# Kernel optimization log

Hardware: AMD Instinct MI355X
Metric: run time of the kernel (lower is better)

## Reference

```python
import jax, jax.numpy as jnp
import numpy as np

N = 50000   # num nodes
E = 800000  # num edges
D = 128     # in_features
C = 1.0     # curvature c
MIN_NORM = 1e-15
BALL_EPS = 4e-3  # float32 boundary eps in PoincareBall.proj


def setup_inputs() -> dict:
    key = jax.random.key(0)
    k1, k2 = jax.random.split(key)
    x = jax.random.normal(k1, (N, D), dtype=jnp.float32)
    edge_index = jax.random.randint(k2, (2, E), 0, N, dtype=jnp.int32)
    return {"x": x, "edge_index": edge_index}


def _expmap0(u, c):
    sqrt_c = c ** 0.5
    u_norm = jnp.maximum(jnp.linalg.norm(u, axis=-1, keepdims=True), MIN_NORM)
    return jnp.tanh(sqrt_c * u_norm) * u / (sqrt_c * u_norm)


def _proj(p, c):
    norm = jnp.maximum(jnp.linalg.norm(p, axis=-1, keepdims=True), MIN_NORM)
    maxnorm = (1.0 - BALL_EPS) / (c ** 0.5)
    return jnp.where(norm > maxnorm, p / norm * maxnorm, p)


def reference(x, edge_index):
    row, col = edge_index[0], edge_index[1]
    # add_remaining_self_loops: drop existing self-loops (weight->0), append N fresh self-loops w=1
    w = jnp.where(row == col, 0.0, 1.0).astype(x.dtype)
    loop = jnp.arange(N, dtype=row.dtype)
    row_f = jnp.concatenate([row, loop])
    col_f = jnp.concatenate([col, loop])
    w_f = jnp.concatenate([w, jnp.ones((N,), x.dtype)])
    # symmetric GCN normalization: D^{-1/2} A D^{-1/2}
    deg = jax.ops.segment_sum(w_f, row_f, num_segments=N)
    dis = jnp.where(deg > 0, 1.0 / jnp.sqrt(jnp.where(deg > 0, deg, 1.0)), 0.0)
    nw = dis[row_f] * w_f * dis[col_f]  # [E+N]
    # gather source features, weighted scatter-add into destination rows
    support = nw[:, None] * x[col_f]                       # [E+N, D]
    result = jax.ops.segment_sum(support, row_f, num_segments=N)  # [N, D]
    return _proj(_expmap0(result, C), C)
```

## Files before the change

### kernel.cpp

```cpp
#include <hip/hip_runtime.h>
#include <math.h>

#define N_NODES 50000
#define N_EDGES 800000
#define DFEAT   128
#define MAXNORM (1.0f - 4e-3f)
#define CAP     64
#define OVF_CAP 8192


__global__ void k_zero(int* __restrict__ deg, int* __restrict__ ovf_cnt, int n) {
    int i = blockIdx.x * blockDim.x + threadIdx.x;
    if (i < n) deg[i] = 0;
    if (i == 0) *ovf_cnt = 0;
}

__global__ void k_build(const int* __restrict__ row, const int* __restrict__ col,
                        int* __restrict__ deg, int* __restrict__ adj,
                        int* __restrict__ ovf, int* __restrict__ ovf_cnt, int e4) {
    int i = blockIdx.x * blockDim.x + threadIdx.x;
    if (i >= e4) return;
    int4 r4 = ((const int4*)row)[i];
    int4 c4 = ((const int4*)col)[i];
    int rs[4] = {r4.x, r4.y, r4.z, r4.w};
    int cs[4] = {c4.x, c4.y, c4.z, c4.w};
    #pragma unroll
    for (int k = 0; k < 4; ++k) {
        int r = rs[k], c = cs[k];
        if (r != c) {
            int pos = atomicAdd(&deg[r], 1);
            if (pos < CAP) adj[r * CAP + pos] = c;
            else {
                int o = atomicAdd(ovf_cnt, 1);
                if (o < OVF_CAP) { ovf[2 * o] = r; ovf[2 * o + 1] = c; }
            }
        }
    }
}

__global__ __launch_bounds__(256) void k_prep(const float* __restrict__ x,
                                              const int* __restrict__ deg,
                                              unsigned int* __restrict__ xb,
                                              int* __restrict__ adj, int nthreads) {
    int t = blockIdx.x * blockDim.x + threadIdx.x;
    if (t >= nthreads) return;

    if (t < N_NODES) {
        int d = deg[t];
        int dcap = d < CAP ? d : CAP;
        int up = (dcap + 3) & ~3;
        for (int p = dcap; p < up; ++p) adj[t * CAP + p] = N_NODES;
    }

    int node = t >> 4;
    int part = t & 15;
    unsigned int w[4];
    if (node < N_NODES) {
        float dis = rsqrtf((float)(deg[node] + 1));
        const float4* x4 = (const float4*)(x + (size_t)node * DFEAT + part * 8);
        float4 a = x4[0];
        float4 b = x4[1];
        float fs[8] = {a.x, a.y, a.z, a.w, b.x, b.y, b.z, b.w};
        #pragma unroll
        for (int k = 0; k < 4; ++k) {
            unsigned int lo = __float_as_uint(fs[2 * k] * dis);
            unsigned int hi = __float_as_uint(fs[2 * k + 1] * dis);
            lo = (lo + 0x7FFFu + ((lo >> 16) & 1u)) >> 16;
            hi = (hi + 0x7FFFu + ((hi >> 16) & 1u)) >> 16;
            w[k] = lo | (hi << 16);
        }
    } else {
        w[0] = w[1] = w[2] = w[3] = 0u;
    }
    ((uint4*)xb)[t] = make_uint4(w[0], w[1], w[2], w[3]);
}

__device__ __forceinline__ float bf_lo(unsigned int w) { return __uint_as_float(w << 16); }
__device__ __forceinline__ float bf_hi(unsigned int w) { return __uint_as_float(w & 0xFFFF0000u); }

__global__ __launch_bounds__(256) void k_gather_bf(const unsigned int* __restrict__ xb,
                                                   const int* __restrict__ adj,
                                                   const int* __restrict__ deg,
                                                   const int* __restrict__ ovf,
                                                   const int* __restrict__ ovf_cnt,
                                                   float* __restrict__ out, int n) {
    int lane = threadIdx.x & 63;
    int rowi = blockIdx.x * 4 + (threadIdx.x >> 6);
    if (rowi >= n) return;

    int cnt    = deg[rowi];
    int capcnt = cnt < CAP ? cnt : CAP;
    int capR   = (capcnt + 3) & ~3;

    int a = N_NODES;
    if (lane < capR) a = adj[rowi * CAP + lane];

    const unsigned int* __restrict__ xl = xb + lane;

    float accx = 0.f, accy = 0.f;
    for (int nb = 0; nb < capR; nb += 4) {
        int c0 = __shfl(a, nb);
        int c1 = __shfl(a, nb + 1);
        int c2 = __shfl(a, nb + 2);
        int c3 = __shfl(a, nb + 3);
        unsigned int v0 = xl[c0 * (DFEAT / 2)];
        unsigned int v1 = xl[c1 * (DFEAT / 2)];
        unsigned int v2 = xl[c2 * (DFEAT / 2)];
        unsigned int v3 = xl[c3 * (DFEAT / 2)];
        accx += bf_lo(v0); accy += bf_hi(v0);
        accx += bf_lo(v1); accy += bf_hi(v1);
        accx += bf_lo(v2); accy += bf_hi(v2);
        accx += bf_lo(v3); accy += bf_hi(v3);
    }

    int novf = *ovf_cnt;
    for (int k = 0; k < novf; ++k) {
        if (ovf[2 * k] == rowi) {
            unsigned int v = xl[ovf[2 * k + 1] * (DFEAT / 2)];
            accx += bf_lo(v); accy += bf_hi(v);
        }
    }

    float di = rsqrtf((float)(cnt + 1));
    unsigned int sv = xl[rowi * (DFEAT / 2)];
    accx = di * (accx + bf_lo(sv));
    accy = di * (accy + bf_hi(sv));

    float nsq = accx * accx + accy * accy;
    #pragma unroll
    for (int off = 32; off > 0; off >>= 1) nsq += __shfl_xor(nsq, off);

    float un = fmaxf(sqrtf(nsq), 1e-15f);
    float th = tanhf(un);
    float scale = th / un;
    if (th > MAXNORM) scale *= MAXNORM / th;

    float2 o = make_float2(accx * scale, accy * scale);
    ((float2*)out)[rowi * (DFEAT / 2) + lane] = o;
}


__global__ __launch_bounds__(256) void k_gather_pad(const float* __restrict__ x,
                                                    const int* __restrict__ adj,
                                                    const int* __restrict__ deg,
                                                    const int* __restrict__ ovf,
                                                    const int* __restrict__ ovf_cnt,
                                                    float* __restrict__ out, int n) {
    int lane = threadIdx.x & 63;
    int rowi = blockIdx.x * 4 + (threadIdx.x >> 6);
    if (rowi >= n) return;

    const float2* __restrict__ x2 = (const float2*)x;
    int cnt    = deg[rowi];
    int capcnt = cnt < CAP ? cnt : CAP;

    int a = 0;
    if (lane < capcnt) a = adj[rowi * CAP + lane];

    float2 acc = make_float2(0.0f, 0.0f);
    for (int nb = 0; nb < capcnt; ++nb) {
        int c = __shfl(a, nb);
        float w = rsqrtf((float)(deg[c] + 1));
        float2 v = x2[c * (DFEAT / 2) + lane];
        acc.x += w * v.x;
        acc.y += w * v.y;
    }

    int novf = *ovf_cnt;
    for (int k = 0; k < novf; ++k) {
        if (ovf[2 * k] == rowi) {
            int c = ovf[2 * k + 1];
            float w = rsqrtf((float)(deg[c] + 1));
            float2 v = x2[c * (DFEAT / 2) + lane];
            acc.x += w * v.x;
            acc.y += w * v.y;
        }
    }

    float di = rsqrtf((float)(cnt + 1));
    float2 self = x2[rowi * (DFEAT / 2) + lane];
    acc.x = di * (acc.x + di * self.x);
    acc.y = di * (acc.y + di * self.y);

    float nsq = acc.x * acc.x + acc.y * acc.y;
    #pragma unroll
    for (int off = 32; off > 0; off >>= 1) nsq += __shfl_xor(nsq, off);

    float un = fmaxf(sqrtf(nsq), 1e-15f);
    float th = tanhf(un);
    float scale = th / un;
    if (th > MAXNORM) scale *= MAXNORM / th;

    float2 o = make_float2(acc.x * scale, acc.y * scale);
    ((float2*)out)[rowi * (DFEAT / 2) + lane] = o;
}


#define SCAN_BLK 256
#define NUM_SCAN_BLOCKS ((N_NODES + SCAN_BLK - 1) / SCAN_BLK)

__global__ void k_init_deg(int* __restrict__ deg, int n) {
    int i = blockIdx.x * blockDim.x + threadIdx.x;
    if (i < n) deg[i] = 1;
}

__global__ void k_hist(const int* __restrict__ row, const int* __restrict__ col,
                       int* __restrict__ deg, int e) {
    int i = blockIdx.x * blockDim.x + threadIdx.x;
    if (i < e) {
        int r = row[i], c = col[i];
        if (r != c) atomicAdd(&deg[r], 1);
    }
}

__global__ __launch_bounds__(SCAN_BLK) void k_block_sums(const int* __restrict__ deg,
                                                         int* __restrict__ blockSums, int n) {
    __shared__ int s[SCAN_BLK];
    int t = threadIdx.x;
    int i = blockIdx.x * SCAN_BLK + t;
    s[t] = (i < n) ? (deg[i] - 1) : 0;
    __syncthreads();
    for (int off = SCAN_BLK / 2; off > 0; off >>= 1) {
        if (t < off) s[t] += s[t + off];
        __syncthreads();
    }
    if (t == 0) blockSums[blockIdx.x] = s[0];
}

__global__ __launch_bounds__(SCAN_BLK) void k_scan_blocks(const int* __restrict__ blockSums,
                                                          int* __restrict__ blockBase) {
    __shared__ int s[SCAN_BLK];
    int t = threadIdx.x;
    s[t] = (t < NUM_SCAN_BLOCKS) ? blockSums[t] : 0;
    __syncthreads();
    for (int off = 1; off < SCAN_BLK; off <<= 1) {
        int v = (t >= off) ? s[t - off] : 0;
        __syncthreads();
        s[t] += v;
        __syncthreads();
    }
    if (t < NUM_SCAN_BLOCKS) blockBase[t] = (t == 0) ? 0 : s[t - 1];
}

__global__ __launch_bounds__(SCAN_BLK) void k_block_scan(const int* __restrict__ deg,
                                                         const int* __restrict__ blockBase,
                                                         int* __restrict__ offs,
                                                         int* __restrict__ cursor, int n) {
    __shared__ int s[SCAN_BLK];
    int t = threadIdx.x;
    int i = blockIdx.x * SCAN_BLK + t;
    int cnt = (i < n) ? (deg[i] - 1) : 0;
    s[t] = cnt;
    __syncthreads();
    for (int off = 1; off < SCAN_BLK; off <<= 1) {
        int v = (t >= off) ? s[t - off] : 0;
        __syncthreads();
        s[t] += v;
        __syncthreads();
    }
    if (i < n) {
        int excl = s[t] - cnt + blockBase[blockIdx.x];
        offs[i]   = excl;
        cursor[i] = excl;
    }
}

__global__ void k_scatter(const int* __restrict__ row, const int* __restrict__ col,
                          int* __restrict__ cursor, int* __restrict__ adj, int e) {
    int i = blockIdx.x * blockDim.x + threadIdx.x;
    if (i < e) {
        int r = row[i], c = col[i];
        if (r != c) {
            int pos = atomicAdd(&cursor[r], 1);
            adj[pos] = c;
        }
    }
}

__global__ __launch_bounds__(256) void k_gather_csr(const float* __restrict__ x,
                                                    const int* __restrict__ adj,
                                                    const int* __restrict__ offs,
                                                    const int* __restrict__ deg,
                                                    float* __restrict__ out, int n) {
    int lane = threadIdx.x & 63;
    int rowi = blockIdx.x * 4 + (threadIdx.x >> 6);
    if (rowi >= n) return;

    const float2* __restrict__ x2 = (const float2*)x;
    int beg = offs[rowi];
    int cnt = deg[rowi] - 1;

    float2 acc = make_float2(0.0f, 0.0f);
    for (int base = 0; base < cnt; base += 64) {
        int m = cnt - base; if (m > 64) m = 64;
        int a = 0;
        if (lane < m) a = adj[beg + base + lane];
        for (int nb = 0; nb < m; ++nb) {
            int c = __shfl(a, nb);
            float w = rsqrtf((float)deg[c]);
            float2 v = x2[c * (DFEAT / 2) + lane];
            acc.x += w * v.x;
            acc.y += w * v.y;
        }
    }
    float di = rsqrtf((float)deg[rowi]);
    float2 self = x2[rowi * (DFEAT / 2) + lane];
    acc.x = di * (acc.x + di * self.x);
    acc.y = di * (acc.y + di * self.y);

    float nsq = acc.x * acc.x + acc.y * acc.y;
    #pragma unroll
    for (int off = 32; off > 0; off >>= 1) nsq += __shfl_xor(nsq, off);

    float un = fmaxf(sqrtf(nsq), 1e-15f);
    float th = tanhf(un);
    float scale = th / un;
    if (th > MAXNORM) scale *= MAXNORM / th;

    float2 o = make_float2(acc.x * scale, acc.y * scale);
    ((float2*)out)[rowi * (DFEAT / 2) + lane] = o;
}


extern "C" void kernel_launch(void* const* d_in, const int* in_sizes, int n_in,
                              void* d_out, int out_size, void* d_ws, size_t ws_size,
                              hipStream_t stream) {
    const float* x          = (const float*)d_in[0];
    const int*   edge_index = (const int*)d_in[1];
    const int*   row = edge_index;
    const int*   col = edge_index + N_EDGES;
    float* out = (float*)d_out;
    char*  ws  = (char*)d_ws;

    size_t sz_xb  = sizeof(unsigned short) * (size_t)(N_NODES + 1) * DFEAT;
    size_t sz_adj = sizeof(int) * (size_t)N_NODES * CAP;
    size_t sz_deg = sizeof(int) * (size_t)N_NODES;
    size_t need_bf  = sz_xb + sz_adj + sz_deg + sizeof(int) * (1 + 2 * (size_t)OVF_CAP);
    size_t need_pad = sz_adj + sz_deg + sizeof(int) * (1 + 2 * (size_t)OVF_CAP);

    dim3 blk(256);
    if (ws_size >= need_bf) {
        size_t off = 0;
        unsigned int* xb = (unsigned int*)(ws + off); off += sz_xb;
        int* adj     = (int*)(ws + off); off += sz_adj;
        int* deg     = (int*)(ws + off); off += sz_deg;
        int* ovf_cnt = (int*)(ws + off); off += sizeof(int);
        int* ovf     = (int*)(ws + off);

        int nprep = (N_NODES + 1) * (DFEAT / 8);
        k_zero<<<dim3((N_NODES + 255) / 256), blk, 0, stream>>>(deg, ovf_cnt, N_NODES);
        k_build<<<dim3((N_EDGES / 4 + 255) / 256), blk, 0, stream>>>(row, col, deg, adj, ovf, ovf_cnt, N_EDGES / 4);
        k_prep<<<dim3((nprep + 255) / 256), blk, 0, stream>>>(x, deg, xb, adj, nprep);
        k_gather_bf<<<dim3((N_NODES + 3) / 4), blk, 0, stream>>>(xb, adj, deg, ovf, ovf_cnt, out, N_NODES);
    } else if (ws_size >= need_pad) {
        size_t off = 0;
        int* adj     = (int*)(ws + off); off += sz_adj;
        int* deg     = (int*)(ws + off); off += sz_deg;
        int* ovf_cnt = (int*)(ws + off); off += sizeof(int);
        int* ovf     = (int*)(ws + off);

        k_zero<<<dim3((N_NODES + 255) / 256), blk, 0, stream>>>(deg, ovf_cnt, N_NODES);
        k_build<<<dim3((N_EDGES / 4 + 255) / 256), blk, 0, stream>>>(row, col, deg, adj, ovf, ovf_cnt, N_EDGES / 4);
        k_gather_pad<<<dim3((N_NODES + 3) / 4), blk, 0, stream>>>(x, adj, deg, ovf, ovf_cnt, out, N_NODES);
    } else {
        size_t off = 0;
        int* deg       = (int*)(ws + off); off += sizeof(int) * (size_t)N_NODES;
        int* offs      = (int*)(ws + off); off += sizeof(int) * (size_t)N_NODES;
        int* cursor    = (int*)(ws + off); off += sizeof(int) * (size_t)N_NODES;
        int* blockSums = (int*)(ws + off); off += sizeof(int) * (size_t)NUM_SCAN_BLOCKS;
        int* blockBase = (int*)(ws + off); off += sizeof(int) * (size_t)NUM_SCAN_BLOCKS;
        int* adj       = (int*)(ws + off);

        k_init_deg<<<dim3((N_NODES + 255) / 256), blk, 0, stream>>>(deg, N_NODES);
        k_hist<<<dim3((N_EDGES + 255) / 256), blk, 0, stream>>>(row, col, deg, N_EDGES);
        k_block_sums<<<dim3(NUM_SCAN_BLOCKS), dim3(SCAN_BLK), 0, stream>>>(deg, blockSums, N_NODES);
        k_scan_blocks<<<dim3(1), dim3(SCAN_BLK), 0, stream>>>(blockSums, blockBase);
        k_block_scan<<<dim3(NUM_SCAN_BLOCKS), dim3(SCAN_BLK), 0, stream>>>(deg, blockBase, offs, cursor, N_NODES);
        k_scatter<<<dim3((N_EDGES + 255) / 256), blk, 0, stream>>>(row, col, cursor, adj, N_EDGES);
        k_gather_csr<<<dim3((N_NODES + 3) / 4), blk, 0, stream>>>(x, adj, offs, deg, out, N_NODES);
    }
}
```

Baseline: 171.1 us.

## Split wavefront into two half-waves each gathering alternate neighbors with 8-byte loads

The gather kernel now has each 32-lane half of the wavefront process alternate neighbors, with each lane loading 4 bf16 features (uint2) instead of 2. The halves are combined with a cross-half shuffle. Padding the adjacency list in k_prep is removed; lanes past the count default to the dummy zero row through the shuffle source. This gives two independent neighbor rows in flight per load instruction and removes a store pass, at the cost of an extra reduction and idle half-wave stores.

```diff
diff --git a/kernel.cpp b/kernel.cpp
--- a/kernel.cpp
+++ b/kernel.cpp
@@ -41,16 +41,9 @@
 __global__ __launch_bounds__(256) void k_prep(const float* __restrict__ x,
                                               const int* __restrict__ deg,
                                               unsigned int* __restrict__ xb,
-                                              int* __restrict__ adj, int nthreads) {
+                                              int nthreads) {
     int t = blockIdx.x * blockDim.x + threadIdx.x;
     if (t >= nthreads) return;
-
-    if (t < N_NODES) {
-        int d = deg[t];
-        int dcap = d < CAP ? d : CAP;
-        int up = (dcap + 3) & ~3;
-        for (int p = dcap; p < up; ++p) adj[t * CAP + p] = N_NODES;
-    }
 
     int node = t >> 4;
     int part = t & 15;
@@ -85,58 +78,72 @@
                                                    const int* __restrict__ ovf_cnt,
                                                    float* __restrict__ out, int n) {
     int lane = threadIdx.x & 63;
+    int half = lane >> 5;
+    int fl   = lane & 31;
     int rowi = blockIdx.x * 4 + (threadIdx.x >> 6);
     if (rowi >= n) return;
 
     int cnt    = deg[rowi];
     int capcnt = cnt < CAP ? cnt : CAP;
-    int capR   = (capcnt + 3) & ~3;
+    int capR   = (capcnt + 7) & ~7;
 
     int a = N_NODES;
-    if (lane < capR) a = adj[rowi * CAP + lane];
-
-    const unsigned int* __restrict__ xl = xb + lane;
-
-    float accx = 0.f, accy = 0.f;
-    for (int nb = 0; nb < capR; nb += 4) {
-        int c0 = __shfl(a, nb);
-        int c1 = __shfl(a, nb + 1);
-        int c2 = __shfl(a, nb + 2);
-        int c3 = __shfl(a, nb + 3);
-        unsigned int v0 = xl[c0 * (DFEAT / 2)];
-        unsigned int v1 = xl[c1 * (DFEAT / 2)];
-        unsigned int v2 = xl[c2 * (DFEAT / 2)];
-        unsigned int v3 = xl[c3 * (DFEAT / 2)];
-        accx += bf_lo(v0); accy += bf_hi(v0);
-        accx += bf_lo(v1); accy += bf_hi(v1);
-        accx += bf_lo(v2); accy += bf_hi(v2);
-        accx += bf_lo(v3); accy += bf_hi(v3);
+    if (lane < capcnt) a = adj[rowi * CAP + lane];
+
+    const unsigned int* __restrict__ xw = xb + 2 * fl;
+
+    float acc0 = 0.f, acc1 = 0.f, acc2 = 0.f, acc3 = 0.f;
+    for (int nb = 0; nb < capR; nb += 8) {
+        int c0 = __shfl(a, nb + 0 + half);
+        int c1 = __shfl(a, nb + 2 + half);
+        int c2 = __shfl(a, nb + 4 + half);
+        int c3 = __shfl(a, nb + 6 + half);
+        uint2 v0 = *(const uint2*)(xw + c0 * (DFEAT / 2));
+        uint2 v1 = *(const uint2*)(xw + c1 * (DFEAT / 2));
+        uint2 v2 = *(const uint2*)(xw + c2 * (DFEAT / 2));
+        uint2 v3 = *(const uint2*)(xw + c3 * (DFEAT / 2));
+        acc0 += bf_lo(v0.x); acc1 += bf_hi(v0.x); acc2 += bf_lo(v0.y); acc3 += bf_hi(v0.y);
+        acc0 += bf_lo(v1.x); acc1 += bf_hi(v1.x); acc2 += bf_lo(v1.y); acc3 += bf_hi(v1.y);
+        acc0 += bf_lo(v2.x); acc1 += bf_hi(v2.x); acc2 += bf_lo(v2.y); acc3 += bf_hi(v2.y);
+        acc0 += bf_lo(v3.x); acc1 += bf_hi(v3.x); acc2 += bf_lo(v3.y); acc3 += bf_hi(v3.y);
     }
 
     int novf = *ovf_cnt;
-    for (int k = 0; k < novf; ++k) {
-        if (ovf[2 * k] == rowi) {
-            unsigned int v = xl[ovf[2 * k + 1] * (DFEAT / 2)];
-            accx += bf_lo(v); accy += bf_hi(v);
-        }
-    }
+    if (novf > 0 && half == 0) {
+        for (int k = 0; k < novf; ++k) {
+            if (ovf[2 * k] == rowi) {
+                uint2 v = *(const uint2*)(xw + ovf[2 * k + 1] * (DFEAT / 2));
+                acc0 += bf_lo(v.x); acc1 += bf_hi(v.x);
+                acc2 += bf_lo(v.y); acc3 += bf_hi(v.y);
+            }
+        }
+    }
+
+    acc0 += __shfl_xor(acc0, 32);
+    acc1 += __shfl_xor(acc1, 32);
+    acc2 += __shfl_xor(acc2, 32);
+    acc3 += __shfl_xor(acc3, 32);
+
+    uint2 sv = *(const uint2*)(xw + rowi * (DFEAT / 2));
+    acc0 += bf_lo(sv.x); acc1 += bf_hi(sv.x);
+    acc2 += bf_lo(sv.y); acc3 += bf_hi(sv.y);
 
     float di = rsqrtf((float)(cnt + 1));
-    unsigned int sv = xl[rowi * (DFEAT / 2)];
-    accx = di * (accx + bf_lo(sv));
-    accy = di * (accy + bf_hi(sv));
-
-    float nsq = accx * accx + accy * accy;
+    acc0 *= di; acc1 *= di; acc2 *= di; acc3 *= di;
+
+    float nsq = acc0 * acc0 + acc1 * acc1 + acc2 * acc2 + acc3 * acc3;
     #pragma unroll
-    for (int off = 32; off > 0; off >>= 1) nsq += __shfl_xor(nsq, off);
+    for (int off = 16; off > 0; off >>= 1) nsq += __shfl_xor(nsq, off);
 
     float un = fmaxf(sqrtf(nsq), 1e-15f);
     float th = tanhf(un);
     float scale = th / un;
     if (th > MAXNORM) scale *= MAXNORM / th;
 
-    float2 o = make_float2(accx * scale, accy * scale);
-    ((float2*)out)[rowi * (DFEAT / 2) + lane] = o;
+    if (half == 0) {
+        float4 o = make_float4(acc0 * scale, acc1 * scale, acc2 * scale, acc3 * scale);
+        *(float4*)(out + (size_t)rowi * DFEAT + 4 * fl) = o;
+    }
 }
 
 
@@ -350,7 +357,7 @@
         int nprep = (N_NODES + 1) * (DFEAT / 8);
         k_zero<<<dim3((N_NODES + 255) / 256), blk, 0, stream>>>(deg, ovf_cnt, N_NODES);
         k_build<<<dim3((N_EDGES / 4 + 255) / 256), blk, 0, stream>>>(row, col, deg, adj, ovf, ovf_cnt, N_EDGES / 4);
-        k_prep<<<dim3((nprep + 255) / 256), blk, 0, stream>>>(x, deg, xb, adj, nprep);
+        k_prep<<<dim3((nprep + 255) / 256), blk, 0, stream>>>(x, deg, xb, nprep);
         k_gather_bf<<<dim3((N_NODES + 3) / 4), blk, 0, stream>>>(xb, adj, deg, ovf, ovf_cnt, out, N_NODES);
     } else if (ws_size >= need_pad) {
         size_t off = 0;
```

Measured after the change: 166.9 us. -2.5%, faster.
